# Kernel tuning notes

Hardware: AMD Instinct MI355X
Metric: run time of the kernel (lower is better)

## Reference

```python
import jax, jax.numpy as jnp
import numpy as np

IN_FEATURES = 4096
OUT_FEATURES = 4096
SHARED_ROWS = 256
BATCH = 8192


def setup_inputs() -> dict:
    key = jax.random.key(0)
    k_x, k_w, k_b = jax.random.split(key, 3)
    x = jax.random.normal(k_x, (BATCH, IN_FEATURES), dtype=jnp.float32)
    shared_weights = jax.random.normal(k_w, (SHARED_ROWS, IN_FEATURES), dtype=jnp.float32)
    bias = jax.random.normal(k_b, (OUT_FEATURES,), dtype=jnp.float32)
    return {"x": x, "shared_weights": shared_weights, "bias": bias}


def reference(x, shared_weights, bias):
    # Faithful to torch: weight_matrix = shared_weights.repeat(out//shared, 1)
    reps = OUT_FEATURES // SHARED_ROWS
    weight_matrix = jnp.tile(shared_weights, (reps, 1))  # [out_features, in_features]
    # y = x @ W^T + b  -> [batch, out_features]
    return jnp.matmul(x, weight_matrix.T) + bias
```

## Files before the change

### kernel.cpp

```cpp
#include <hip/hip_runtime.h>
#include <cstdint>
#include <cstddef>

#define M_DIM 8192
#define N_DIM 256
#define K_DIM 4096
#define OUT_F 4096
#define BM 64
#define BK 64
#define NTH 512
#define LDK 72

typedef float    float4_  __attribute__((ext_vector_type(4)));
typedef _Float16 half8    __attribute__((ext_vector_type(8)));
typedef _Float16 half4    __attribute__((ext_vector_type(4)));
typedef unsigned int uint4_ __attribute__((ext_vector_type(4)));

__global__ __launch_bounds__(256) void convert_w_kernel(const float* __restrict__ w,
                                                        _Float16* __restrict__ wh) {
  int i = (blockIdx.x * 256 + threadIdx.x) * 8;
  float4_ f0 = *(const float4_*)(w + i);
  float4_ f1 = *(const float4_*)(w + i + 4);
  half8 h;
  h[0] = (_Float16)f0[0]; h[1] = (_Float16)f0[1];
  h[2] = (_Float16)f0[2]; h[3] = (_Float16)f0[3];
  h[4] = (_Float16)f1[0]; h[5] = (_Float16)f1[1];
  h[6] = (_Float16)f1[2]; h[7] = (_Float16)f1[3];
  *(half8*)(wh + i) = h;
}

__global__ __launch_bounds__(NTH, 4) void gemm_s_kernel(const float* __restrict__ x,
                                                        const _Float16* __restrict__ wh,
                                                        float* __restrict__ P,
                                                        int nkt) {
  __shared__ __align__(16) _Float16 As[BM][LDK];
  __shared__ __align__(16) _Float16 Bs[N_DIM][LDK];

  const int tid  = threadIdx.x;
  const int wv   = tid >> 6;
  const int lane = tid & 63;
  const int quad = lane >> 4;
  const int l16  = lane & 15;
  const int mw   = wv >> 2;
  const int n0   = (wv & 3) * 64;
  const int m0   = blockIdx.x * BM;
  const int kbase = blockIdx.y * nkt * BK;

  const int arow = tid >> 3;
  const int acol = (tid & 7) * 8;
  const float* xg = x + (size_t)(m0 + arow) * K_DIM + kbase + acol;
  const _Float16* wgb = wh + (size_t)arow * K_DIM + kbase + acol;

  float4_ acc[2][4];
  const float4_ fzero = {0.f, 0.f, 0.f, 0.f};
#pragma unroll
  for (int i = 0; i < 2; ++i)
#pragma unroll
    for (int j = 0; j < 4; ++j) acc[i][j] = fzero;

  float4_ aPre0 = *(const float4_*)(xg);
  float4_ aPre1 = *(const float4_*)(xg + 4);
  uint4_ bPre[4];
#pragma unroll
  for (int p = 0; p < 4; ++p)
    bPre[p] = *(const uint4_*)(wgb + (size_t)p * 64 * K_DIM);

  for (int kt = 0; kt < nkt; ++kt) {
    half8 ah;
    ah[0] = (_Float16)aPre0[0]; ah[1] = (_Float16)aPre0[1];
    ah[2] = (_Float16)aPre0[2]; ah[3] = (_Float16)aPre0[3];
    ah[4] = (_Float16)aPre1[0]; ah[5] = (_Float16)aPre1[1];
    ah[6] = (_Float16)aPre1[2]; ah[7] = (_Float16)aPre1[3];
    *(half8*)(&As[arow][acol]) = ah;
#pragma unroll
    for (int p = 0; p < 4; ++p)
      *(uint4_*)(&Bs[p * 64 + arow][acol]) = bPre[p];
    __syncthreads();

    if (kt + 1 < nkt) {
      const int k1 = (kt + 1) * BK;
      aPre0 = *(const float4_*)(xg + k1);
      aPre1 = *(const float4_*)(xg + k1 + 4);
#pragma unroll
      for (int p = 0; p < 4; ++p)
        bPre[p] = *(const uint4_*)(wgb + (size_t)p * 64 * K_DIM + k1);
    }

#pragma unroll
    for (int ks = 0; ks < 2; ++ks) {
      const int koff = ks * 32 + quad * 8;
      half8 a0 = *(const half8*)(&As[mw * 32 + l16][koff]);
      half8 a1 = *(const half8*)(&As[mw * 32 + 16 + l16][koff]);
      half8 b0 = *(const half8*)(&Bs[n0 + l16][koff]);
      half8 b1 = *(const half8*)(&Bs[n0 + 16 + l16][koff]);
      half8 b2 = *(const half8*)(&Bs[n0 + 32 + l16][koff]);
      half8 b3 = *(const half8*)(&Bs[n0 + 48 + l16][koff]);
      acc[0][0] = __builtin_amdgcn_mfma_f32_16x16x32_f16(a0, b0, acc[0][0], 0, 0, 0);
      acc[1][0] = __builtin_amdgcn_mfma_f32_16x16x32_f16(a1, b0, acc[1][0], 0, 0, 0);
      acc[0][1] = __builtin_amdgcn_mfma_f32_16x16x32_f16(a0, b1, acc[0][1], 0, 0, 0);
      acc[1][1] = __builtin_amdgcn_mfma_f32_16x16x32_f16(a1, b1, acc[1][1], 0, 0, 0);
      acc[0][2] = __builtin_amdgcn_mfma_f32_16x16x32_f16(a0, b2, acc[0][2], 0, 0, 0);
      acc[1][2] = __builtin_amdgcn_mfma_f32_16x16x32_f16(a1, b2, acc[1][2], 0, 0, 0);
      acc[0][3] = __builtin_amdgcn_mfma_f32_16x16x32_f16(a0, b3, acc[0][3], 0, 0, 0);
      acc[1][3] = __builtin_amdgcn_mfma_f32_16x16x32_f16(a1, b3, acc[1][3], 0, 0, 0);
    }
    __syncthreads();
  }

  float* Pout = P + (size_t)blockIdx.y * (M_DIM * N_DIM);
  const int mbase = m0 + mw * 32 + quad * 4;
  const int nbase = n0 + l16;
#pragma unroll
  for (int mf = 0; mf < 2; ++mf)
#pragma unroll
    for (int nf = 0; nf < 4; ++nf)
#pragma unroll
      for (int r = 0; r < 4; ++r)
        Pout[(size_t)(mbase + mf * 16 + r) * N_DIM + nbase + nf * 16] = acc[mf][nf][r];
}

__global__ __launch_bounds__(256) void expand_kernel(const float* __restrict__ P,
                                                     const float* __restrict__ bias,
                                                     float* __restrict__ out,
                                                     int nks) {
  __shared__ __align__(16) float bsh[OUT_F];
  const int tid = threadIdx.x;
  const float4_* b4 = (const float4_*)bias;
  float4_* bs4 = (float4_*)bsh;
#pragma unroll
  for (int p = 0; p < 4; ++p) bs4[p * 256 + tid] = b4[p * 256 + tid];
  __syncthreads();

  const int ml  = tid >> 6;
  const int c64 = tid & 63;
  const float4_* P4 = (const float4_*)P;

#pragma unroll
  for (int pass = 0; pass < 2; ++pass) {
    const int m = blockIdx.x * 8 + pass * 4 + ml;
    float4_ s = {0.f, 0.f, 0.f, 0.f};
    for (int ks = 0; ks < nks; ++ks)
      s += P4[((size_t)ks * M_DIM + m) * (N_DIM / 4) + c64];
    float4_* orow = (float4_*)(out + (size_t)m * OUT_F);
#pragma unroll
    for (int c = 0; c < 16; ++c)
      orow[c * 64 + c64] = s + bs4[c * 64 + c64];
  }
}

extern "C" void kernel_launch(void* const* d_in, const int* in_sizes, int n_in,
                              void* d_out, int out_size, void* d_ws, size_t ws_size,
                              hipStream_t stream) {
  const float* x    = (const float*)d_in[0];
  const float* w    = (const float*)d_in[1];
  const float* bias = (const float*)d_in[2];
  float* out        = (float*)d_out;
  _Float16* wh      = (_Float16*)d_ws;
  float* P          = (float*)((char*)d_ws + (2u << 20));

  const size_t whB    = (size_t)N_DIM * K_DIM * 2;
  const size_t pslice = (size_t)M_DIM * N_DIM * 4;
  int KS = (ws_size >= whB + 4 * pslice) ? 4
         : (ws_size >= whB + 2 * pslice) ? 2 : 1;
  int nkt = (K_DIM / BK) / KS;

  convert_w_kernel<<<(N_DIM * K_DIM) / (256 * 8), 256, 0, stream>>>(w, wh);
  gemm_s_kernel<<<dim3(M_DIM / BM, KS), NTH, 0, stream>>>(x, wh, P, nkt);
  expand_kernel<<<M_DIM / 8, 256, 0, stream>>>(P, bias, out, KS);
}
```

Baseline: 271.3 us.

## Fuse GEMM and tiled bias expansion into one kernel, loading W fragments directly

Replaces the split-K GEMM plus separate expand kernel with one fused kernel. Each block computes a 32-row tile over all of K, stages the result in shared memory, then writes the 16x replicated output with the bias added, using nontemporal stores. The partial-sum buffer and its extra global round trip go away. Weight fragments are now read straight from global or L2 into registers instead of through LDS, and A is double-buffered in LDS. The cost is no split-K parallelism (256 blocks), heavy repeated weight traffic from L2, and larger shared memory per block.

```diff
diff --git a/kernel.cpp b/kernel.cpp
--- a/kernel.cpp
+++ b/kernel.cpp
@@ -6,7 +6,7 @@
 #define N_DIM 256
 #define K_DIM 4096
 #define OUT_F 4096
-#define BM 64
+#define BM 32
 #define BK 64
 #define NTH 512
 #define LDK 72
@@ -14,7 +14,6 @@
 typedef float    float4_  __attribute__((ext_vector_type(4)));
 typedef _Float16 half8    __attribute__((ext_vector_type(8)));
 typedef _Float16 half4    __attribute__((ext_vector_type(4)));
-typedef unsigned int uint4_ __attribute__((ext_vector_type(4)));
 
 __global__ __launch_bounds__(256) void convert_w_kernel(const float* __restrict__ w,
                                                         _Float16* __restrict__ wh) {
@@ -29,122 +28,127 @@
   *(half8*)(wh + i) = h;
 }
 
-__global__ __launch_bounds__(NTH, 4) void gemm_s_kernel(const float* __restrict__ x,
-                                                        const _Float16* __restrict__ wh,
-                                                        float* __restrict__ P,
-                                                        int nkt) {
-  __shared__ __align__(16) _Float16 As[BM][LDK];
-  __shared__ __align__(16) _Float16 Bs[N_DIM][LDK];
+__device__ __forceinline__ void load_bfrag(half8 b[2][2],
+                                           const _Float16* __restrict__ wg0,
+                                           const _Float16* __restrict__ wg1,
+                                           int kk) {
+#pragma unroll
+  for (int ks = 0; ks < 2; ++ks) {
+    b[ks][0] = *(const half8*)(wg0 + kk + ks * 32);
+    b[ks][1] = *(const half8*)(wg1 + kk + ks * 32);
+  }
+}
+
+__device__ __forceinline__ void stage_a(_Float16 (*As)[LDK], int arow, int acol,
+                                        float4_ a) {
+  half4 h;
+  h[0] = (_Float16)a[0]; h[1] = (_Float16)a[1];
+  h[2] = (_Float16)a[2]; h[3] = (_Float16)a[3];
+  *(half4*)(&As[arow][acol]) = h;
+}
+
+__device__ __forceinline__ void mfma_step(float4_ acc[2][2], const half8 b[2][2],
+                                          const _Float16 (*As)[LDK],
+                                          int l16, int quad) {
+#pragma unroll
+  for (int ks = 0; ks < 2; ++ks) {
+    const int koff = ks * 32 + quad * 8;
+    half8 a0 = *(const half8*)(&As[l16][koff]);
+    half8 a1 = *(const half8*)(&As[16 + l16][koff]);
+    acc[0][0] = __builtin_amdgcn_mfma_f32_16x16x32_f16(a0, b[ks][0], acc[0][0], 0, 0, 0);
+    acc[1][0] = __builtin_amdgcn_mfma_f32_16x16x32_f16(a1, b[ks][0], acc[1][0], 0, 0, 0);
+    acc[0][1] = __builtin_amdgcn_mfma_f32_16x16x32_f16(a0, b[ks][1], acc[0][1], 0, 0, 0);
+    acc[1][1] = __builtin_amdgcn_mfma_f32_16x16x32_f16(a1, b[ks][1], acc[1][1], 0, 0, 0);
+  }
+}
+
+__global__ __launch_bounds__(NTH, 2) void fused_kernel(const float* __restrict__ x,
+                                                       const _Float16* __restrict__ wh,
+                                                       const float* __restrict__ bias,
+                                                       float* __restrict__ out) {
+  __shared__ __align__(16) _Float16 As[2][BM][LDK];
+  __shared__ __align__(16) float Ssh[BM][N_DIM + 4];
+  __shared__ __align__(16) float bsh[OUT_F];
 
   const int tid  = threadIdx.x;
   const int wv   = tid >> 6;
   const int lane = tid & 63;
   const int quad = lane >> 4;
   const int l16  = lane & 15;
-  const int mw   = wv >> 2;
-  const int n0   = (wv & 3) * 64;
+  const int n0   = wv * 32;
   const int m0   = blockIdx.x * BM;
-  const int kbase = blockIdx.y * nkt * BK;
 
-  const int arow = tid >> 3;
-  const int acol = (tid & 7) * 8;
-  const float* xg = x + (size_t)(m0 + arow) * K_DIM + kbase + acol;
-  const _Float16* wgb = wh + (size_t)arow * K_DIM + kbase + acol;
+  {
+    const float4_* b4 = (const float4_*)bias;
+    float4_* bs4 = (float4_*)bsh;
+    bs4[tid] = b4[tid];
+    bs4[NTH + tid] = b4[NTH + tid];
+  }
 
-  float4_ acc[2][4];
+  const int arow = tid >> 4;
+  const int acol = (tid & 15) * 4;
+  const float* xg = x + (size_t)(m0 + arow) * K_DIM + acol;
+
+  const _Float16* wg0 = wh + (size_t)(n0 + l16) * K_DIM + quad * 8;
+  const _Float16* wg1 = wg0 + (size_t)16 * K_DIM;
+
+  float4_ acc[2][2];
   const float4_ fzero = {0.f, 0.f, 0.f, 0.f};
 #pragma unroll
   for (int i = 0; i < 2; ++i)
 #pragma unroll
-    for (int j = 0; j < 4; ++j) acc[i][j] = fzero;
+    for (int j = 0; j < 2; ++j) acc[i][j] = fzero;
 
-  float4_ aPre0 = *(const float4_*)(xg);
-  float4_ aPre1 = *(const float4_*)(xg + 4);
-  uint4_ bPre[4];
-#pragma unroll
-  for (int p = 0; p < 4; ++p)
-    bPre[p] = *(const uint4_*)(wgb + (size_t)p * 64 * K_DIM);
+  half8 bA[2][2], bB[2][2];
+  float4_ aP0 = __builtin_nontemporal_load((const float4_*)(xg));
+  float4_ aP1 = __builtin_nontemporal_load((const float4_*)(xg + BK));
+  load_bfrag(bA, wg0, wg1, 0);
+  stage_a(As[0], arow, acol, aP0);
+  aP0 = __builtin_nontemporal_load((const float4_*)(xg + 2 * BK));
+  __syncthreads();
 
-  for (int kt = 0; kt < nkt; ++kt) {
-    half8 ah;
-    ah[0] = (_Float16)aPre0[0]; ah[1] = (_Float16)aPre0[1];
-    ah[2] = (_Float16)aPre0[2]; ah[3] = (_Float16)aPre0[3];
-    ah[4] = (_Float16)aPre1[0]; ah[5] = (_Float16)aPre1[1];
-    ah[6] = (_Float16)aPre1[2]; ah[7] = (_Float16)aPre1[3];
-    *(half8*)(&As[arow][acol]) = ah;
-#pragma unroll
-    for (int p = 0; p < 4; ++p)
-      *(uint4_*)(&Bs[p * 64 + arow][acol]) = bPre[p];
+  const int NKT = K_DIM / BK;
+  for (int kt = 0; kt < NKT; kt += 2) {
+    load_bfrag(bB, wg0, wg1, (kt + 1) * BK);
+    stage_a(As[1], arow, acol, aP1);
+    if (kt + 3 < NKT)
+      aP1 = __builtin_nontemporal_load((const float4_*)(xg + (kt + 3) * BK));
+    mfma_step(acc, bA, As[0], l16, quad);
     __syncthreads();
 
-    if (kt + 1 < nkt) {
-      const int k1 = (kt + 1) * BK;
-      aPre0 = *(const float4_*)(xg + k1);
-      aPre1 = *(const float4_*)(xg + k1 + 4);
-#pragma unroll
-      for (int p = 0; p < 4; ++p)
-        bPre[p] = *(const uint4_*)(wgb + (size_t)p * 64 * K_DIM + k1);
+    if (kt + 2 < NKT) {
+      load_bfrag(bA, wg0, wg1, (kt + 2) * BK);
+      stage_a(As[0], arow, acol, aP0);
+      if (kt + 4 < NKT)
+        aP0 = __builtin_nontemporal_load((const float4_*)(xg + (kt + 4) * BK));
     }
-
-#pragma unroll
-    for (int ks = 0; ks < 2; ++ks) {
-      const int koff = ks * 32 + quad * 8;
-      half8 a0 = *(const half8*)(&As[mw * 32 + l16][koff]);
-      half8 a1 = *(const half8*)(&As[mw * 32 + 16 + l16][koff]);
-      half8 b0 = *(const half8*)(&Bs[n0 + l16][koff]);
-      half8 b1 = *(const half8*)(&Bs[n0 + 16 + l16][koff]);
-      half8 b2 = *(const half8*)(&Bs[n0 + 32 + l16][koff]);
-      half8 b3 = *(const half8*)(&Bs[n0 + 48 + l16][koff]);
-      acc[0][0] = __builtin_amdgcn_mfma_f32_16x16x32_f16(a0, b0, acc[0][0], 0, 0, 0);
-      acc[1][0] = __builtin_amdgcn_mfma_f32_16x16x32_f16(a1, b0, acc[1][0], 0, 0, 0);
-      acc[0][1] = __builtin_amdgcn_mfma_f32_16x16x32_f16(a0, b1, acc[0][1], 0, 0, 0);
-      acc[1][1] = __builtin_amdgcn_mfma_f32_16x16x32_f16(a1, b1, acc[1][1], 0, 0, 0);
-      acc[0][2] = __builtin_amdgcn_mfma_f32_16x16x32_f16(a0, b2, acc[0][2], 0, 0, 0);
-      acc[1][2] = __builtin_amdgcn_mfma_f32_16x16x32_f16(a1, b2, acc[1][2], 0, 0, 0);
-      acc[0][3] = __builtin_amdgcn_mfma_f32_16x16x32_f16(a0, b3, acc[0][3], 0, 0, 0);
-      acc[1][3] = __builtin_amdgcn_mfma_f32_16x16x32_f16(a1, b3, acc[1][3], 0, 0, 0);
-    }
+    mfma_step(acc, bB, As[1], l16, quad);
     __syncthreads();
   }
 
-  float* Pout = P + (size_t)blockIdx.y * (M_DIM * N_DIM);
-  const int mbase = m0 + mw * 32 + quad * 4;
-  const int nbase = n0 + l16;
 #pragma unroll
   for (int mf = 0; mf < 2; ++mf)
 #pragma unroll
-    for (int nf = 0; nf < 4; ++nf)
+    for (int nf = 0; nf < 2; ++nf)
 #pragma unroll
       for (int r = 0; r < 4; ++r)
-        Pout[(size_t)(mbase + mf * 16 + r) * N_DIM + nbase + nf * 16] = acc[mf][nf][r];
-}
-
-__global__ __launch_bounds__(256) void expand_kernel(const float* __restrict__ P,
-                                                     const float* __restrict__ bias,
-                                                     float* __restrict__ out,
-                                                     int nks) {
-  __shared__ __align__(16) float bsh[OUT_F];
-  const int tid = threadIdx.x;
-  const float4_* b4 = (const float4_*)bias;
-  float4_* bs4 = (float4_*)bsh;
-#pragma unroll
-  for (int p = 0; p < 4; ++p) bs4[p * 256 + tid] = b4[p * 256 + tid];
+        Ssh[mf * 16 + quad * 4 + r][n0 + nf * 16 + l16] = acc[mf][nf][r];
   __syncthreads();
 
-  const int ml  = tid >> 6;
-  const int c64 = tid & 63;
-  const float4_* P4 = (const float4_*)P;
+  float4_ s[4];
+#pragma unroll
+  for (int rr = 0; rr < 4; ++rr)
+    s[rr] = *(const float4_*)(&Ssh[wv * 4 + rr][lane * 4]);
 
+  float4_* o0 = (float4_*)(out + (size_t)(m0 + wv * 4) * OUT_F);
+  const float4_* bs4 = (const float4_*)bsh;
 #pragma unroll
-  for (int pass = 0; pass < 2; ++pass) {
-    const int m = blockIdx.x * 8 + pass * 4 + ml;
-    float4_ s = {0.f, 0.f, 0.f, 0.f};
-    for (int ks = 0; ks < nks; ++ks)
-      s += P4[((size_t)ks * M_DIM + m) * (N_DIM / 4) + c64];
-    float4_* orow = (float4_*)(out + (size_t)m * OUT_F);
+  for (int i = 0; i < 16; ++i) {
+    float4_ b4 = bs4[i * 64 + lane];
 #pragma unroll
-    for (int c = 0; c < 16; ++c)
-      orow[c * 64 + c64] = s + bs4[c * 64 + c64];
+    for (int rr = 0; rr < 4; ++rr)
+      __builtin_nontemporal_store(s[rr] + b4,
+                                  o0 + (size_t)rr * (OUT_F / 4) + i * 64 + lane);
   }
 }
 
@@ -156,15 +160,7 @@
   const float* bias = (const float*)d_in[2];
   float* out        = (float*)d_out;
   _Float16* wh      = (_Float16*)d_ws;
-  float* P          = (float*)((char*)d_ws + (2u << 20));
-
-  const size_t whB    = (size_t)N_DIM * K_DIM * 2;
-  const size_t pslice = (size_t)M_DIM * N_DIM * 4;
-  int KS = (ws_size >= whB + 4 * pslice) ? 4
-         : (ws_size >= whB + 2 * pslice) ? 2 : 1;
-  int nkt = (K_DIM / BK) / KS;
 
   convert_w_kernel<<<(N_DIM * K_DIM) / (256 * 8), 256, 0, stream>>>(w, wh);
-  gemm_s_kernel<<<dim3(M_DIM / BM, KS), NTH, 0, stream>>>(x, wh, P, nkt);
-  expand_kernel<<<M_DIM / 8, 256, 0, stream>>>(P, bias, out, KS);
+  fused_kernel<<<M_DIM / BM, NTH, 0, stream>>>(x, wh, bias, out);
 }
```

New measurement: 278.2 us. 2.5% more time.
